# Kernel tuning notes

Hardware: AMD Instinct MI355X
Metric: run time of the kernel (lower is better)

## Reference

```python
import jax, jax.numpy as jnp
import numpy as np

B, N, W, H = 2, 2048, 1024, 16
HD = W // H  # head dim = 64
STD = 0.02


def setup_inputs() -> dict:
    key = jax.random.key(0)
    ks = jax.random.split(key, 8)
    x = jax.random.normal(ks[0], (B, N, W), dtype=jnp.float32)
    # weights stored [in, out] (transposed vs torch nn.Linear)
    qkv_w = jax.random.normal(ks[1], (W, 3 * W), dtype=jnp.float32) * STD
    qkv_b = jnp.zeros((3 * W,), jnp.float32)
    proj_w = jax.random.normal(ks[2], (W, W), dtype=jnp.float32) * STD
    proj_b = jnp.zeros((W,), jnp.float32)
    fc_w = jax.random.normal(ks[3], (W, 4 * W), dtype=jnp.float32) * STD
    fc_b = jnp.zeros((4 * W,), jnp.float32)
    fc2_w = jax.random.normal(ks[4], (4 * W, W), dtype=jnp.float32) * STD
    fc2_b = jnp.zeros((W,), jnp.float32)
    ln1_g = jnp.ones((W,), jnp.float32)
    ln1_b = jnp.zeros((W,), jnp.float32)
    ln2_g = jnp.ones((W,), jnp.float32)
    ln2_b = jnp.zeros((W,), jnp.float32)
    return dict(x=x, ln1_g=ln1_g, ln1_b=ln1_b, qkv_w=qkv_w, qkv_b=qkv_b,
                proj_w=proj_w, proj_b=proj_b, ln2_g=ln2_g, ln2_b=ln2_b,
                fc_w=fc_w, fc_b=fc_b, fc2_w=fc2_w, fc2_b=fc2_b)


def _layernorm(x, g, b, eps=1e-5):
    mu = jnp.mean(x, axis=-1, keepdims=True)
    var = jnp.var(x, axis=-1, keepdims=True)
    return (x - mu) * jax.lax.rsqrt(var + eps) * g + b


def _attention(x, qkv_w, qkv_b, proj_w, proj_b):
    bs, n, w = x.shape
    qkv = x @ qkv_w + qkv_b                      # [b, n, 3W]
    qkv = qkv.reshape(bs, n, H, 3 * HD)
    q, k, v = jnp.split(qkv, 3, axis=-1)         # each [b, n, h, hd]
    scale = 1.0 / np.sqrt(np.sqrt(HD)).astype(np.float32)
    # hand-rolled attention: full [b, h, t, s] score matrix, fp32 softmax
    weight = jnp.einsum('bthc,bshc->bhts', q * scale, k * scale)
    weight = jax.nn.softmax(weight.astype(jnp.float32), axis=-1).astype(weight.dtype)
    out = jnp.einsum('bhts,bshc->bthc', weight, v).reshape(bs, n, w)
    return out @ proj_w + proj_b


def reference(x, ln1_g, ln1_b, qkv_w, qkv_b, proj_w, proj_b,
              ln2_g, ln2_b, fc_w, fc_b, fc2_w, fc2_b):
    x = x + _attention(_layernorm(x, ln1_g, ln1_b), qkv_w, qkv_b, proj_w, proj_b)
    h = _layernorm(x, ln2_g, ln2_b)
    h = jax.nn.gelu(h @ fc_w + fc_b, approximate=False) @ fc2_w + fc2_b
    return x + h
```

## Files before the change

### kernel.cpp

```cpp
#include <hip/hip_runtime.h>
#include <hip/hip_bf16.h>
#include <type_traits>
#include <cstdint>

using bf16 = __hip_bfloat16;
typedef __attribute__((ext_vector_type(8))) short bf16x8;
typedef __attribute__((ext_vector_type(4))) float f32x4;

__device__ __forceinline__ float bf2f(unsigned short u) {
    union { unsigned int i; float f; } c; c.i = ((unsigned int)u) << 16; return c.f;
}

__device__ __forceinline__ float gelu_f(float v) {
    float x  = v * 0.70710678118654752f;
    float ax = fabsf(x);
    float t  = __builtin_amdgcn_rcpf(1.0f + 0.3275911f * ax);
    float poly = ((((1.061405429f * t - 1.453152027f) * t + 1.421413741f) * t
                   - 0.284496736f) * t + 0.254829592f) * t;
    float erfv = 1.0f - poly * __expf(-ax * ax);
    erfv = copysignf(erfv, x);
    return 0.5f * v * (1.0f + erfv);
}

#define GLLDS16(gp, lp)                                                          \
    __builtin_amdgcn_global_load_lds(                                            \
        (const __attribute__((address_space(1))) void*)(gp),                     \
        (__attribute__((address_space(3))) void*)(lp), 16, 0, 0)

__global__ __launch_bounds__(256) void transpose_f2b(const float* __restrict__ w,
                                                     bf16* __restrict__ wt,
                                                     int K, int N) {
    __shared__ bf16 t[32][33];
    const int tid = threadIdx.x;
    const int n0 = blockIdx.x * 32, k0 = blockIdx.y * 32;
#pragma unroll
    for (int i = 0; i < 4; ++i) {
        int idx = tid + i * 256;
        int r = idx >> 5, c = idx & 31;
        t[r][c] = __float2bfloat16(w[(size_t)(k0 + r) * N + n0 + c]);
    }
    __syncthreads();
#pragma unroll
    for (int i = 0; i < 4; ++i) {
        int idx = tid + i * 256;
        int r = idx >> 5, c = idx & 31;
        wt[(size_t)(n0 + r) * K + k0 + c] = t[c][r];
    }
}

__global__ __launch_bounds__(256) void vtrans_kernel(const bf16* __restrict__ qkv,
                                                     bf16* __restrict__ vtg) {
    __shared__ bf16 t[32][33];
    const int tid = threadIdx.x;
    const int s0 = blockIdx.x * 32, c0 = blockIdx.y * 32;
    const int bh = blockIdx.z, b = bh >> 4, h = bh & 15;
#pragma unroll
    for (int i = 0; i < 4; ++i) {
        int idx = tid + i * 256;
        int r = idx >> 5, c = idx & 31;
        t[r][c] = qkv[(size_t)(b * 2048 + s0 + r) * 3072 + h * 192 + 128 + c0 + c];
    }
    __syncthreads();
#pragma unroll
    for (int i = 0; i < 4; ++i) {
        int idx = tid + i * 256;
        int r = idx >> 5, c = idx & 31;
        vtg[((size_t)bh * 64 + c0 + r) * 2048 + s0 + c] = t[c][r];
    }
}

template <typename InT>
__global__ __launch_bounds__(256) void ln_kernel(const InT* __restrict__ x,
                                                 const float* __restrict__ g,
                                                 const float* __restrict__ bta,
                                                 bf16* __restrict__ y) {
    const int row = blockIdx.x, tid = threadIdx.x;
    const size_t base = (size_t)row * 1024 + tid * 4;
    float v[4];
    if constexpr (std::is_same_v<InT, float>) {
        float4 f = *(const float4*)(x + base);
        v[0] = f.x; v[1] = f.y; v[2] = f.z; v[3] = f.w;
    } else {
        ushort4 u = *(const ushort4*)((const unsigned short*)x + base);
        v[0] = bf2f(u.x); v[1] = bf2f(u.y); v[2] = bf2f(u.z); v[3] = bf2f(u.w);
    }
    float s = v[0] + v[1] + v[2] + v[3];
    float sq = v[0]*v[0] + v[1]*v[1] + v[2]*v[2] + v[3]*v[3];
#pragma unroll
    for (int off = 32; off > 0; off >>= 1) {
        s  += __shfl_down(s, off);
        sq += __shfl_down(sq, off);
    }
    __shared__ float red[8];
    const int wave = tid >> 6, lane = tid & 63;
    if (lane == 0) { red[wave] = s; red[4 + wave] = sq; }
    __syncthreads();
    s  = red[0] + red[1] + red[2] + red[3];
    sq = red[4] + red[5] + red[6] + red[7];
    const float mu   = s * (1.0f / 1024.0f);
    const float var  = sq * (1.0f / 1024.0f) - mu * mu;
    const float rstd = rsqrtf(var + 1e-5f);
#pragma unroll
    for (int e = 0; e < 4; ++e) {
        int col = tid * 4 + e;
        float yy = (v[e] - mu) * rstd * g[col] + bta[col];
        y[base + e] = __float2bfloat16(yy);
    }
}

template <int EPI, int BM, bool XSWZ>
__global__ __launch_bounds__(256) void gemm_kernel(const bf16* __restrict__ A,
                                                   const bf16* __restrict__ Bt,
                                                   const float* __restrict__ bias,
                                                   const void* __restrict__ resid,
                                                   void* __restrict__ Cout,
                                                   int M, int N, int K) {
    constexpr int IF = 4;
    constexpr int JF = (BM == 128) ? 4 : 2;
    constexpr bool GL = (BM == 128);
    constexpr int ST = GL ? 64 : 72;
    constexpr int NB = GL ? 2 : 1;
    __shared__ __align__(16) bf16 As[NB][BM * ST];
    __shared__ __align__(16) bf16 Bs[NB][128 * ST];
    const int tid  = threadIdx.x;
    const int wave = tid >> 6, lane = tid & 63;
    const int quad = lane >> 4, l16 = lane & 15;
    const int wm = GL ? (wave >> 1) * 64 : 0;
    const int wn = GL ? (wave & 1) * 64 : wave * 32;

    int bx = blockIdx.x, by = blockIdx.y, bz = blockIdx.z;
    if constexpr (XSWZ) {
        const int gx = gridDim.x, gy = gridDim.y;
        const int nwg = gx * gy * gridDim.z;
        const int f = bx + gx * (by + gy * bz);
        const int s = (f & 7) * (nwg >> 3) + (f >> 3);
        bx = s % gx; int rem = s / gx; by = rem % gy; bz = rem / gy;
    }
    const int bm = by * BM, bn = bx * 128;

    int kz0 = 0, kz1 = K;
    if constexpr (EPI == 4) {
        kz0 = bz * (K >> 1);
        kz1 = kz0 + (K >> 1);
    }

    const int r8 = lane >> 3, sc = lane & 7;
    const bf16* ag = A  + (size_t)(bm + wave * 8 + r8) * K + ((sc ^ r8) << 3);
    const bf16* bg = Bt + (size_t)(bn + wave * 8 + r8) * K + ((sc ^ r8) << 3);

    f32x4 acc[IF][JF];
#pragma unroll
    for (int i = 0; i < IF; ++i)
#pragma unroll
        for (int j = 0; j < JF; ++j) acc[i][j] = (f32x4){0.f, 0.f, 0.f, 0.f};

    if constexpr (GL) {
        auto stage = [&](int buf, int kt) {
#pragma unroll
            for (int i = 0; i < 4; ++i) {
                GLLDS16(ag + (size_t)(i * 32) * K + kt, &As[buf][(wave * 8 + i * 32) * 64]);
                GLLDS16(bg + (size_t)(i * 32) * K + kt, &Bs[buf][(wave * 8 + i * 32) * 64]);
            }
        };
        auto compute = [&](int buf) {
#pragma unroll
            for (int ks = 0; ks < 2; ++ks) {
                bf16x8 af[IF], bfr[JF];
                const int swr = l16 & 7;
#pragma unroll
                for (int i = 0; i < IF; ++i)
                    af[i] = *(const bf16x8*)(&As[buf][(wm + i * 16 + l16) * 64 +
                                                      (((ks * 4 + quad) ^ swr) << 3)]);
#pragma unroll
                for (int j = 0; j < JF; ++j)
                    bfr[j] = *(const bf16x8*)(&Bs[buf][(wn + j * 16 + l16) * 64 +
                                                       (((ks * 4 + quad) ^ swr) << 3)]);
#pragma unroll
                for (int i = 0; i < IF; ++i)
#pragma unroll
                    for (int j = 0; j < JF; ++j)
                        acc[i][j] = __builtin_amdgcn_mfma_f32_16x16x32_bf16(af[i], bfr[j], acc[i][j], 0, 0, 0);
            }
        };
        stage(0, kz0);
        __syncthreads();
        int cur = 0;
        for (int kt = kz0; kt < kz1; kt += 64) {
            if (kt + 64 < kz1) stage(cur ^ 1, kt + 64);
            compute(cur);
            __syncthreads();
            cur ^= 1;
        }
    } else {
        for (int kt = kz0; kt < kz1; kt += 64) {
            __syncthreads();
#pragma unroll
            for (int i = 0; i < BM * 8 / 256; ++i) {
                int c0 = tid + i * 256;
                int r = c0 >> 3, kc = (c0 & 7) << 3;
                *(uint4*)(&As[0][r * ST + kc]) = *(const uint4*)(A + (size_t)(bm + r) * K + kt + kc);
            }
#pragma unroll
            for (int i = 0; i < 4; ++i) {
                int c0 = tid + i * 256;
                int r = c0 >> 3, kc = (c0 & 7) << 3;
                *(uint4*)(&Bs[0][r * ST + kc]) = *(const uint4*)(Bt + (size_t)(bn + r) * K + kt + kc);
            }
            __syncthreads();
#pragma unroll
            for (int ks = 0; ks < 2; ++ks) {
                bf16x8 af[IF], bfr[JF];
#pragma unroll
                for (int i = 0; i < IF; ++i)
                    af[i] = *(const bf16x8*)(&As[0][(wm + i * 16 + l16) * ST + ks * 32 + quad * 8]);
#pragma unroll
                for (int j = 0; j < JF; ++j)
                    bfr[j] = *(const bf16x8*)(&Bs[0][(wn + j * 16 + l16) * ST + ks * 32 + quad * 8]);
#pragma unroll
                for (int i = 0; i < IF; ++i)
#pragma unroll
                    for (int j = 0; j < JF; ++j)
                        acc[i][j] = __builtin_amdgcn_mfma_f32_16x16x32_bf16(af[i], bfr[j], acc[i][j], 0, 0, 0);
            }
        }
    }
    float* skdst = nullptr;
    if constexpr (EPI == 4)
        skdst = bz ? (float*)const_cast<void*>(resid) : (float*)Cout;
#pragma unroll
    for (int i = 0; i < IF; ++i) {
#pragma unroll
        for (int j = 0; j < JF; ++j) {
#pragma unroll
            for (int r = 0; r < 4; ++r) {
                const int row = bm + wm + i * 16 + quad * 4 + r;
                const int col = bn + wn + j * 16 + l16;
                float v = acc[i][j][r];
                if constexpr (EPI != 4) v += bias[col];
                if constexpr (EPI == 1)
                    v = gelu_f(v);
                if constexpr (EPI == 2) {
                    v += ((const float*)resid)[(size_t)row * N + col];
                    ((bf16*)Cout)[(size_t)row * N + col] = __float2bfloat16(v);
                } else if constexpr (EPI == 3) {
                    v += bf2f(((const unsigned short*)resid)[(size_t)row * N + col]);
                    ((float*)Cout)[(size_t)row * N + col] = v;
                } else if constexpr (EPI == 4) {
                    skdst[(size_t)row * N + col] = v;
                } else {
                    ((bf16*)Cout)[(size_t)row * N + col] = __float2bfloat16(v);
                }
            }
        }
    }
}

__global__ __launch_bounds__(256) void merge_fc2(const float* __restrict__ p0,
                                                 const float* __restrict__ p1,
                                                 const float* __restrict__ bias,
                                                 const bf16* __restrict__ resid,
                                                 float* __restrict__ outp) {
    const int idx = blockIdx.x * 256 + threadIdx.x;
    const int row = idx >> 8, col = (idx & 255) * 4;
    const size_t off = (size_t)row * 1024 + col;
    float4 a = *(const float4*)(p0 + off);
    float4 b = *(const float4*)(p1 + off);
    float4 bs = *(const float4*)(bias + col);
    ushort4 r = *(const ushort4*)((const unsigned short*)resid + off);
    float4 o;
    o.x = a.x + b.x + bs.x + bf2f(r.x);
    o.y = a.y + b.y + bs.y + bf2f(r.y);
    o.z = a.z + b.z + bs.z + bf2f(r.z);
    o.w = a.w + b.w + bs.w + bf2f(r.w);
    *(float4*)(outp + off) = o;
}

__global__ __launch_bounds__(256) void attn_kernel(const bf16* __restrict__ qkv,
                                                   const bf16* __restrict__ vtg,
                                                   bf16* __restrict__ Opart,
                                                   float* __restrict__ Lp) {
    __shared__ __align__(16) bf16 Ks[64 * 64];
    __shared__ __align__(16) bf16 Vs[64 * 64];
    __shared__ __align__(16) bf16 Ps[4][2][16][72];
    const int tid  = threadIdx.x;
    const int wave = tid >> 6, lane = tid & 63;
    const int quad = lane >> 4, l16 = lane & 15;
    const int f = blockIdx.x + 16 * blockIdx.y + 256 * blockIdx.z;
    const int sid = (f & 7) * 128 + (f >> 3);
    const int qt = sid & 15, h = (sid >> 4) & 15;
    const int zz = sid >> 8;
    const int b = zz >> 1, seg = zz & 1;
    const size_t tok0 = (size_t)b * 2048;
    const int qbase = qt * 128 + wave * 32;

    bf16x8 qf[2][2];
#pragma unroll
    for (int set = 0; set < 2; ++set) {
        const bf16* qp = qkv + (tok0 + qbase + set * 16 + l16) * 3072 + h * 192 + quad * 8;
        qf[set][0] = *(const bf16x8*)(qp);
        qf[set][1] = *(const bf16x8*)(qp + 32);
    }

    const int swc = ((tid & 7) ^ ((tid >> 3) & 7)) * 8;
    const bf16* kg = qkv + (tok0 + (tid >> 3)) * 3072 + h * 192 + 64 + swc;
    const bf16* vg = vtg + ((size_t)(b * 16 + h) * 64 + (tid >> 3)) * 2048 + swc;

    const short oneb = 0x3f80;
    const bf16x8 ones = {oneb, oneb, oneb, oneb, oneb, oneb, oneb, oneb};

    f32x4 o[2][4], l_acc[2];
#pragma unroll
    for (int set = 0; set < 2; ++set) {
        l_acc[set] = (f32x4){0.f, 0.f, 0.f, 0.f};
#pragma unroll
        for (int j = 0; j < 4; ++j) o[set][j] = (f32x4){0.f, 0.f, 0.f, 0.f};
    }

    const int kt0 = seg * 1024;
    for (int kt = kt0; kt < kt0 + 1024; kt += 64) {
        __syncthreads();
        GLLDS16(kg + (size_t)kt * 3072,        &Ks[(wave * 64) * 8]);
        GLLDS16(kg + (size_t)(kt + 32) * 3072, &Ks[(wave * 64 + 256) * 8]);
        GLLDS16(vg + kt,                       &Vs[(wave * 64) * 8]);
        GLLDS16(vg + kt + 32 * 2048,           &Vs[(wave * 64 + 256) * 8]);
        __syncthreads();

#pragma unroll
        for (int j = 0; j < 4; ++j) {
            const int rk = j * 16 + l16;
            const int sw = l16 & 7;
            bf16x8 kb0 = *(const bf16x8*)(&Ks[rk * 64 + ((quad ^ sw) * 8)]);
            bf16x8 kb1 = *(const bf16x8*)(&Ks[rk * 64 + (((quad + 4) ^ sw) * 8)]);
#pragma unroll
            for (int set = 0; set < 2; ++set) {
                f32x4 s4 = (f32x4){0.f, 0.f, 0.f, 0.f};
                s4 = __builtin_amdgcn_mfma_f32_16x16x32_bf16(qf[set][0], kb0, s4, 0, 0, 0);
                s4 = __builtin_amdgcn_mfma_f32_16x16x32_bf16(qf[set][1], kb1, s4, 0, 0, 0);
#pragma unroll
                for (int r = 0; r < 4; ++r)
                    Ps[wave][set][quad * 4 + r][j * 16 + l16] =
                        __float2bfloat16(__expf(s4[r] * 0.125f));
            }
        }
#pragma unroll
        for (int kk = 0; kk < 2; ++kk) {
            bf16x8 pf0 = *(const bf16x8*)(&Ps[wave][0][l16][kk * 32 + quad * 8]);
            bf16x8 pf1 = *(const bf16x8*)(&Ps[wave][1][l16][kk * 32 + quad * 8]);
            l_acc[0] = __builtin_amdgcn_mfma_f32_16x16x32_bf16(pf0, ones, l_acc[0], 0, 0, 0);
            l_acc[1] = __builtin_amdgcn_mfma_f32_16x16x32_bf16(pf1, ones, l_acc[1], 0, 0, 0);
#pragma unroll
            for (int j = 0; j < 4; ++j) {
                const int rv = j * 16 + l16;
                bf16x8 vf = *(const bf16x8*)(&Vs[rv * 64 + (((kk * 4 + quad) ^ (l16 & 7)) * 8)]);
                o[0][j] = __builtin_amdgcn_mfma_f32_16x16x32_bf16(pf0, vf, o[0][j], 0, 0, 0);
                o[1][j] = __builtin_amdgcn_mfma_f32_16x16x32_bf16(pf1, vf, o[1][j], 0, 0, 0);
            }
        }
    }
    const size_t segoff = (size_t)seg * 4096;
#pragma unroll
    for (int set = 0; set < 2; ++set)
#pragma unroll
        for (int j = 0; j < 4; ++j)
#pragma unroll
            for (int r = 0; r < 4; ++r) {
                int row = qbase + set * 16 + quad * 4 + r;
                Opart[(segoff + tok0 + row) * 1024 + h * 64 + j * 16 + l16] =
                    __float2bfloat16(o[set][j][r]);
            }
    if (l16 == 0) {
#pragma unroll
        for (int set = 0; set < 2; ++set)
#pragma unroll
            for (int r = 0; r < 4; ++r) {
                int row = qbase + set * 16 + quad * 4 + r;
                Lp[(segoff + tok0 + row) * 16 + h] = l_acc[set][r];
            }
    }
}

__global__ __launch_bounds__(256) void merge_kernel(const bf16* __restrict__ Opart,
                                                    const float* __restrict__ Lp,
                                                    bf16* __restrict__ outp) {
    const int idx = blockIdx.x * 256 + threadIdx.x;
    const int c4 = idx & 15, h = (idx >> 4) & 15, gt = idx >> 8;
    const size_t li0 = (size_t)gt * 16 + h, li1 = li0 + 4096 * 16;
    float inv = 1.0f / (Lp[li0] + Lp[li1]);
    const size_t off = (size_t)gt * 1024 + h * 64 + c4 * 4;
    ushort4 a = *(const ushort4*)((const unsigned short*)Opart + off);
    ushort4 bb = *(const ushort4*)((const unsigned short*)Opart + off + (size_t)4096 * 1024);
    float va[4] = {bf2f(a.x), bf2f(a.y), bf2f(a.z), bf2f(a.w)};
    float vb[4] = {bf2f(bb.x), bf2f(bb.y), bf2f(bb.z), bf2f(bb.w)};
    unsigned short res[4];
#pragma unroll
    for (int e = 0; e < 4; ++e) {
        bf16 o = __float2bfloat16((va[e] + vb[e]) * inv);
        res[e] = *(unsigned short*)&o;
    }
    *(ushort4*)((unsigned short*)outp + off) = make_ushort4(res[0], res[1], res[2], res[3]);
}

extern "C" void kernel_launch(void* const* d_in, const int* in_sizes, int n_in,
                              void* d_out, int out_size, void* d_ws, size_t ws_size,
                              hipStream_t stream) {
    const float* x      = (const float*)d_in[0];
    const float* ln1_g  = (const float*)d_in[1];
    const float* ln1_b  = (const float*)d_in[2];
    const float* qkv_w  = (const float*)d_in[3];
    const float* qkv_b  = (const float*)d_in[4];
    const float* proj_w = (const float*)d_in[5];
    const float* proj_b = (const float*)d_in[6];
    const float* ln2_g  = (const float*)d_in[7];
    const float* ln2_b  = (const float*)d_in[8];
    const float* fc_w   = (const float*)d_in[9];
    const float* fc_b   = (const float*)d_in[10];
    const float* fc2_w  = (const float*)d_in[11];
    const float* fc2_b  = (const float*)d_in[12];
    float* outp = (float*)d_out;

    char* ws = (char*)d_ws;
    const size_t MB = 1024 * 1024;
    bf16*  wfcT   = (bf16*)(ws + 0 * MB);
    float* part1  = (float*)(ws + 0 * MB);
    bf16*  lnbuf  = (bf16*)(ws + 8 * MB);
    bf16*  wprojT = (bf16*)(ws + 8 * MB);
    float* Lp     = (float*)(ws + 10 * MB);
    bf16*  wqkvT  = (bf16*)(ws + 16 * MB);
    bf16*  vtg    = (bf16*)(ws + 16 * MB);
    bf16*  attnout= (bf16*)(ws + 16 * MB);
    bf16*  fcact  = (bf16*)(ws + 16 * MB);
    bf16*  qkvb   = (bf16*)(ws + 24 * MB);
    bf16*  Opart  = (bf16*)(ws + 48 * MB);
    bf16*  wfc2T  = (bf16*)(ws + 48 * MB);
    bf16*  x1     = (bf16*)(ws + 56 * MB);

    transpose_f2b<<<dim3(96, 32),  256, 0, stream>>>(qkv_w, wqkvT, 1024, 3072);
    transpose_f2b<<<dim3(128, 32), 256, 0, stream>>>(fc_w,  wfcT,  1024, 4096);
    ln_kernel<float><<<4096, 256, 0, stream>>>(x, ln1_g, ln1_b, lnbuf);
    gemm_kernel<0, 128, false><<<dim3(24, 32), 256, 0, stream>>>(lnbuf, wqkvT, qkv_b, nullptr, qkvb, 4096, 3072, 1024);
    vtrans_kernel<<<dim3(64, 2, 32), 256, 0, stream>>>(qkvb, vtg);
    transpose_f2b<<<dim3(32, 32), 256, 0, stream>>>(proj_w, wprojT, 1024, 1024);
    attn_kernel<<<dim3(16, 16, 4), 256, 0, stream>>>(qkvb, vtg, Opart, Lp);
    merge_kernel<<<4096, 256, 0, stream>>>(Opart, Lp, attnout);
    transpose_f2b<<<dim3(32, 128), 256, 0, stream>>>(fc2_w, wfc2T, 4096, 1024);
    gemm_kernel<2, 64, true><<<dim3(8, 64), 256, 0, stream>>>(attnout, wprojT, proj_b, x, x1, 4096, 1024, 1024);
    ln_kernel<bf16><<<4096, 256, 0, stream>>>(x1, ln2_g, ln2_b, lnbuf);
    gemm_kernel<1, 128, false><<<dim3(32, 32), 256, 0, stream>>>(lnbuf, wfcT, fc_b, nullptr, fcact, 4096, 4096, 1024);
    gemm_kernel<4, 64, true><<<dim3(8, 64, 2), 256, 0, stream>>>(fcact, wfc2T, nullptr, part1, outp, 4096, 1024, 4096);
    merge_fc2<<<4096, 256, 0, stream>>>(outp, part1, fc2_b, x1, outp);
}
```

Measured before the change: 370.8 us.

## Replace split-K fc2 GEMM with 64x64 tiles and fused residual epilogue

Drops the split-K path for the fc2 GEMM, which wrote two fp32 partial sums and then combined them in a separate merge kernel. fc2 now runs as a single-pass GEMM on 64x64 tiles, with bias and residual added in the epilogue. The proj GEMM also moves to 64x64 tiles, giving each GEMM 1024 workgroups. This removes the partial-sum traffic and one launch, but each workgroup now walks the full K=4096 with small tiles and a single LDS buffer, so reuse per load is lower.

```diff
diff --git a/kernel.cpp b/kernel.cpp
--- a/kernel.cpp
+++ b/kernel.cpp
@@ -108,41 +108,35 @@
     }
 }
 
-template <int EPI, int BM, bool XSWZ>
+template <int EPI, int BM, int BN, bool XSWZ>
 __global__ __launch_bounds__(256) void gemm_kernel(const bf16* __restrict__ A,
                                                    const bf16* __restrict__ Bt,
                                                    const float* __restrict__ bias,
                                                    const void* __restrict__ resid,
                                                    void* __restrict__ Cout,
                                                    int M, int N, int K) {
-    constexpr int IF = 4;
+    constexpr bool GL = (BM == 128);
+    constexpr int IF = (BM == 128) ? 4 : (BN == 128 ? 4 : 2);
     constexpr int JF = (BM == 128) ? 4 : 2;
-    constexpr bool GL = (BM == 128);
     constexpr int ST = GL ? 64 : 72;
     constexpr int NB = GL ? 2 : 1;
     __shared__ __align__(16) bf16 As[NB][BM * ST];
-    __shared__ __align__(16) bf16 Bs[NB][128 * ST];
+    __shared__ __align__(16) bf16 Bs[NB][BN * ST];
     const int tid  = threadIdx.x;
     const int wave = tid >> 6, lane = tid & 63;
     const int quad = lane >> 4, l16 = lane & 15;
-    const int wm = GL ? (wave >> 1) * 64 : 0;
-    const int wn = GL ? (wave & 1) * 64 : wave * 32;
-
-    int bx = blockIdx.x, by = blockIdx.y, bz = blockIdx.z;
+    const int wm = (BM == 128) ? (wave >> 1) * 64 : (BN == 64 ? (wave >> 1) * 32 : 0);
+    const int wn = (BM == 128) ? (wave & 1) * 64 : (BN == 64 ? (wave & 1) * 32 : wave * 32);
+
+    int bx = blockIdx.x, by = blockIdx.y;
     if constexpr (XSWZ) {
         const int gx = gridDim.x, gy = gridDim.y;
-        const int nwg = gx * gy * gridDim.z;
-        const int f = bx + gx * (by + gy * bz);
+        const int nwg = gx * gy;
+        const int f = bx + gx * by;
         const int s = (f & 7) * (nwg >> 3) + (f >> 3);
-        bx = s % gx; int rem = s / gx; by = rem % gy; bz = rem / gy;
-    }
-    const int bm = by * BM, bn = bx * 128;
-
-    int kz0 = 0, kz1 = K;
-    if constexpr (EPI == 4) {
-        kz0 = bz * (K >> 1);
-        kz1 = kz0 + (K >> 1);
-    }
+        bx = s % gx; by = s / gx;
+    }
+    const int bm = by * BM, bn = bx * BN;
 
     const int r8 = lane >> 3, sc = lane & 7;
     const bf16* ag = A  + (size_t)(bm + wave * 8 + r8) * K + ((sc ^ r8) << 3);
@@ -182,17 +176,17 @@
                         acc[i][j] = __builtin_amdgcn_mfma_f32_16x16x32_bf16(af[i], bfr[j], acc[i][j], 0, 0, 0);
             }
         };
-        stage(0, kz0);
+        stage(0, 0);
         __syncthreads();
         int cur = 0;
-        for (int kt = kz0; kt < kz1; kt += 64) {
-            if (kt + 64 < kz1) stage(cur ^ 1, kt + 64);
+        for (int kt = 0; kt < K; kt += 64) {
+            if (kt + 64 < K) stage(cur ^ 1, kt + 64);
             compute(cur);
             __syncthreads();
             cur ^= 1;
         }
     } else {
-        for (int kt = kz0; kt < kz1; kt += 64) {
+        for (int kt = 0; kt < K; kt += 64) {
             __syncthreads();
 #pragma unroll
             for (int i = 0; i < BM * 8 / 256; ++i) {
@@ -201,7 +195,7 @@
                 *(uint4*)(&As[0][r * ST + kc]) = *(const uint4*)(A + (size_t)(bm + r) * K + kt + kc);
             }
 #pragma unroll
-            for (int i = 0; i < 4; ++i) {
+            for (int i = 0; i < BN * 8 / 256; ++i) {
                 int c0 = tid + i * 256;
                 int r = c0 >> 3, kc = (c0 & 7) << 3;
                 *(uint4*)(&Bs[0][r * ST + kc]) = *(const uint4*)(Bt + (size_t)(bn + r) * K + kt + kc);
@@ -224,9 +218,6 @@
             }
         }
     }
-    float* skdst = nullptr;
-    if constexpr (EPI == 4)
-        skdst = bz ? (float*)const_cast<void*>(resid) : (float*)Cout;
 #pragma unroll
     for (int i = 0; i < IF; ++i) {
 #pragma unroll
@@ -235,8 +226,7 @@
             for (int r = 0; r < 4; ++r) {
                 const int row = bm + wm + i * 16 + quad * 4 + r;
                 const int col = bn + wn + j * 16 + l16;
-                float v = acc[i][j][r];
-                if constexpr (EPI != 4) v += bias[col];
+                float v = acc[i][j][r] + bias[col];
                 if constexpr (EPI == 1)
                     v = gelu_f(v);
                 if constexpr (EPI == 2) {
@@ -245,34 +235,12 @@
                 } else if constexpr (EPI == 3) {
                     v += bf2f(((const unsigned short*)resid)[(size_t)row * N + col]);
                     ((float*)Cout)[(size_t)row * N + col] = v;
-                } else if constexpr (EPI == 4) {
-                    skdst[(size_t)row * N + col] = v;
                 } else {
                     ((bf16*)Cout)[(size_t)row * N + col] = __float2bfloat16(v);
                 }
             }
         }
     }
-}
-
-__global__ __launch_bounds__(256) void merge_fc2(const float* __restrict__ p0,
-                                                 const float* __restrict__ p1,
-                                                 const float* __restrict__ bias,
-                                                 const bf16* __restrict__ resid,
-                                                 float* __restrict__ outp) {
-    const int idx = blockIdx.x * 256 + threadIdx.x;
-    const int row = idx >> 8, col = (idx & 255) * 4;
-    const size_t off = (size_t)row * 1024 + col;
-    float4 a = *(const float4*)(p0 + off);
-    float4 b = *(const float4*)(p1 + off);
-    float4 bs = *(const float4*)(bias + col);
-    ushort4 r = *(const ushort4*)((const unsigned short*)resid + off);
-    float4 o;
-    o.x = a.x + b.x + bs.x + bf2f(r.x);
-    o.y = a.y + b.y + bs.y + bf2f(r.y);
-    o.z = a.z + b.z + bs.z + bf2f(r.z);
-    o.w = a.w + b.w + bs.w + bf2f(r.w);
-    *(float4*)(outp + off) = o;
 }
 
 __global__ __launch_bounds__(256) void attn_kernel(const bf16* __restrict__ qkv,
@@ -421,7 +389,6 @@
     char* ws = (char*)d_ws;
     const size_t MB = 1024 * 1024;
     bf16*  wfcT   = (bf16*)(ws + 0 * MB);
-    float* part1  = (float*)(ws + 0 * MB);
     bf16*  lnbuf  = (bf16*)(ws + 8 * MB);
     bf16*  wprojT = (bf16*)(ws + 8 * MB);
     float* Lp     = (float*)(ws + 10 * MB);
@@ -437,15 +404,14 @@
     transpose_f2b<<<dim3(96, 32),  256, 0, stream>>>(qkv_w, wqkvT, 1024, 3072);
     transpose_f2b<<<dim3(128, 32), 256, 0, stream>>>(fc_w,  wfcT,  1024, 4096);
     ln_kernel<float><<<4096, 256, 0, stream>>>(x, ln1_g, ln1_b, lnbuf);
-    gemm_kernel<0, 128, false><<<dim3(24, 32), 256, 0, stream>>>(lnbuf, wqkvT, qkv_b, nullptr, qkvb, 4096, 3072, 1024);
+    gemm_kernel<0, 128, 128, false><<<dim3(24, 32), 256, 0, stream>>>(lnbuf, wqkvT, qkv_b, nullptr, qkvb, 4096, 3072, 1024);
     vtrans_kernel<<<dim3(64, 2, 32), 256, 0, stream>>>(qkvb, vtg);
     transpose_f2b<<<dim3(32, 32), 256, 0, stream>>>(proj_w, wprojT, 1024, 1024);
     attn_kernel<<<dim3(16, 16, 4), 256, 0, stream>>>(qkvb, vtg, Opart, Lp);
     merge_kernel<<<4096, 256, 0, stream>>>(Opart, Lp, attnout);
     transpose_f2b<<<dim3(32, 128), 256, 0, stream>>>(fc2_w, wfc2T, 4096, 1024);
-    gemm_kernel<2, 64, true><<<dim3(8, 64), 256, 0, stream>>>(attnout, wprojT, proj_b, x, x1, 4096, 1024, 1024);
+    gemm_kernel<2, 64, 64, true><<<dim3(16, 64), 256, 0, stream>>>(attnout, wprojT, proj_b, x, x1, 4096, 1024, 1024);
     ln_kernel<bf16><<<4096, 256, 0, stream>>>(x1, ln2_g, ln2_b, lnbuf);
-    gemm_kernel<1, 128, false><<<dim3(32, 32), 256, 0, stream>>>(lnbuf, wfcT, fc_b, nullptr, fcact, 4096, 4096, 1024);
-    gemm_kernel<4, 64, true><<<dim3(8, 64, 2), 256, 0, stream>>>(fcact, wfc2T, nullptr, part1, outp, 4096, 1024, 4096);
-    merge_fc2<<<4096, 256, 0, stream>>>(outp, part1, fc2_b, x1, outp);
-}
+    gemm_kernel<1, 128, 128, false><<<dim3(32, 32), 256, 0, stream>>>(lnbuf, wfcT, fc_b, nullptr, fcact, 4096, 4096, 1024);
+    gemm_kernel<3, 64, 64, true><<<dim3(16, 64), 256, 0, stream>>>(fcact, wfc2T, fc2_b, x1, outp, 4096, 1024, 4096);
+}
```

Result: slower. 418.8 us (+12.9%).
